# Performance work log

Hardware: AMD Instinct MI355X
Metric: run time of the kernel (lower is better)

Reference implementation:

```python
import jax, jax.numpy as jnp
import numpy as np

NUM_HEADS = 16
ROPE_BASE = 10000.0


def _rope_tables(head_dim, seq_len, dtype=jnp.float32):
    # Half-split convention: rotate first half against second half.
    inv_freq = 1.0 / (ROPE_BASE ** (jnp.arange(0, head_dim, 2, dtype=dtype) / head_dim))
    pos = jnp.arange(seq_len, dtype=dtype)
    angles_half = jnp.einsum('s,d->sd', pos, inv_freq)          # (S, D/2)
    angles = jnp.concatenate([angles_half, angles_half], -1)     # (S, D)
    return jnp.cos(angles), jnp.sin(angles)


def _apply_rope(x, cos, sin):
    # x: (H, S, D); cos/sin: (S, D) broadcast over heads
    half = x.shape[-1] // 2
    x1, x2 = x[..., :half], x[..., half:]
    x_rot = jnp.concatenate([-x2, x1], axis=-1)
    return x * cos + x_rot * sin


def setup_inputs() -> dict:
    key = jax.random.key(0)
    S, E = 2048, 2048
    ks = jax.random.split(key, 9)
    sc = 0.02
    return {
        'x': jax.random.normal(ks[0], (S, E), jnp.float32),
        'Wq': jax.random.normal(ks[1], (E, E), jnp.float32) * sc,
        'bq': jax.random.normal(ks[2], (E,), jnp.float32) * sc,
        'Wk': jax.random.normal(ks[3], (E, E), jnp.float32) * sc,
        'bk': jax.random.normal(ks[4], (E,), jnp.float32) * sc,
        'Wv': jax.random.normal(ks[5], (E, E), jnp.float32) * sc,
        'bv': jax.random.normal(ks[6], (E,), jnp.float32) * sc,
        'Wo': jax.random.normal(ks[7], (E, E), jnp.float32) * sc,
        'bo': jax.random.normal(ks[8], (E,), jnp.float32) * sc,
    }


def reference(x, Wq, bq, Wk, bk, Wv, bv, Wo, bo):
    S, E = x.shape
    H = NUM_HEADS
    D = E // H
    scale = D ** 0.5
    cos, sin = _rope_tables(D, S, x.dtype)

    def proj(W, b):
        return (x @ W.T + b).reshape(S, H, D).transpose(1, 0, 2)  # (H, S, D)

    q = _apply_rope(proj(Wq, bq), cos, sin)
    k = _apply_rope(proj(Wk, bk), cos, sin)
    v = proj(Wv, bv)

    scores = jnp.einsum('hsd,htd->hst', q, k) / scale  # (H, S, S)
    attn = jax.nn.softmax(scores, axis=-1)
    out = jnp.einsum('hst,htd->hsd', attn, v)          # (H, S, D)
    # Faithful to the original's transpose(0,1).view(S,E) on a (1,H,S,D)
    # tensor: an in-order (head-major) flatten reinterpreted as (S, E).
    out = out.reshape(S, E)
    return out @ Wo.T + bo
```

## Files before the change

kernel.cpp:

```cpp
#include <hip/hip_runtime.h>

#define SDIM 2048
#define EDIM 2048
#define NHEAD 16
#define DHEAD 128

typedef __attribute__((ext_vector_type(8))) short short8;
typedef __attribute__((ext_vector_type(4))) float floatx4;

__device__ __forceinline__ float bf2f(ushort u) {
    union { uint i; float f; } v; v.i = ((uint)u) << 16; return v.f;
}
__device__ __forceinline__ ushort f2bf(float f) {
    union { float f; uint i; } v; v.f = f;
    uint r = v.i + 0x7fff + ((v.i >> 16) & 1);
    return (ushort)(r >> 16);
}

__device__ __forceinline__ void gload_lds16(const ushort* g, ushort* l) {
    __builtin_amdgcn_global_load_lds(
        (const __attribute__((address_space(1))) void*)g,
        (__attribute__((address_space(3))) void*)l, 16, 0, 0);
}

__global__ void convert5_kernel(
    const float* __restrict__ s0, const float* __restrict__ s1,
    const float* __restrict__ s2, const float* __restrict__ s3,
    const float* __restrict__ s4,
    ushort* __restrict__ d0, ushort* __restrict__ d1,
    ushort* __restrict__ d2, ushort* __restrict__ d3,
    ushort* __restrict__ d4)
{
    const float* src; ushort* dst;
    switch (blockIdx.y) {
        case 0: src = s0; dst = d0; break;
        case 1: src = s1; dst = d1; break;
        case 2: src = s2; dst = d2; break;
        case 3: src = s3; dst = d3; break;
        default: src = s4; dst = d4; break;
    }
    int i = blockIdx.x * blockDim.x + threadIdx.x;
    float4 f = ((const float4*)src)[i];
    ushort4 o;
    o.x = f2bf(f.x); o.y = f2bf(f.y); o.z = f2bf(f.z); o.w = f2bf(f.w);
    ((ushort4*)dst)[i] = o;
}

#define QPRESCALE 0.12754245f
__global__ void rope_kernel(ushort* __restrict__ Q, ushort* __restrict__ K) {
    int t = blockIdx.x * blockDim.x + threadIdx.x;
    int arr = t >> 18;
    int r = t & 0x3FFFF;
    int g = r & 7;
    int h = (r >> 3) & 15;
    int s = r >> 7;
    ushort* P = arr ? K : Q;
    float qsc = arr ? 1.0f : QPRESCALE;
    size_t base = ((size_t)s << 11) + (h << 7) + g * 8;
    union { uint4 v; ushort u[8]; } x1, x2, o1, o2;
    x1.v = *(const uint4*)(P + base);
    x2.v = *(const uint4*)(P + base + 64);
    float fs = (float)s;
#pragma unroll
    for (int j = 0; j < 8; j++) {
        int i = g * 8 + j;
        float inv = __expf((float)i * -0.14391157f);
        float ang = fs * inv;
        float rev = ang * 0.15915494309f;
        rev = rev - floorf(rev);
        float ar = rev * 6.28318530718f;
        float sn = __sinf(ar), cs = __cosf(ar);
        float a = bf2f(x1.u[j]), b = bf2f(x2.u[j]);
        o1.u[j] = f2bf((a * cs - b * sn) * qsc);
        o2.u[j] = f2bf((b * cs + a * sn) * qsc);
    }
    *(uint4*)(P + base) = o1.v;
    *(uint4*)(P + base + 64) = o2.v;
}

__device__ __forceinline__ void stout(float* p, float v)  { *p = v; }
__device__ __forceinline__ void stout(ushort* p, float v) { *p = f2bf(v); }

template <typename OUTT>
__global__ __launch_bounds__(256) void gemm_bt(
    const ushort* __restrict__ A,
    const ushort* __restrict__ B0, const ushort* __restrict__ B1, const ushort* __restrict__ B2,
    const float* __restrict__ s0, const float* __restrict__ s1, const float* __restrict__ s2,
    OUTT* __restrict__ C0, OUTT* __restrict__ C1, OUTT* __restrict__ C2,
    int nbpm, int vt_which)
{
    __shared__ __align__(16) ushort a_s[128 * 32];
    __shared__ __align__(16) ushort b_s[128 * 32];

    const int tid = threadIdx.x;
    const int wave = tid >> 6, lane = tid & 63;
    const int l15 = lane & 15, quad = lane >> 4;
    const int wm = wave & 1, wn = wave >> 1;
    const int bm = blockIdx.x * 128;
    const int which = blockIdx.y / nbpm;
    const int n0 = (blockIdx.y % nbpm) * 128;

    const ushort* B   = (which == 0) ? B0 : (which == 1) ? B1 : B2;
    const float*  bia = (which == 0) ? s0 : (which == 1) ? s1 : s2;
    OUTT*         C   = (which == 0) ? C0 : (which == 1) ? C1 : C2;

    floatx4 acc[4][4];
#pragma unroll
    for (int i = 0; i < 4; i++)
#pragma unroll
        for (int j = 0; j < 4; j++) acc[i][j] = (floatx4)0.0f;

    const int t1 = tid + 256;
    const int row0 = tid >> 2, kc0 = (tid & 3) * 8;
    const int row1 = t1 >> 2,  kc1 = (t1 & 3) * 8;

    for (int k0 = 0; k0 < EDIM; k0 += 32) {
        __syncthreads();
        gload_lds16(A + (size_t)(bm + row0) * EDIM + k0 + kc0, a_s + tid * 8);
        gload_lds16(A + (size_t)(bm + row1) * EDIM + k0 + kc1, a_s + t1 * 8);
        gload_lds16(B + (size_t)(n0 + row0) * EDIM + k0 + kc0, b_s + tid * 8);
        gload_lds16(B + (size_t)(n0 + row1) * EDIM + k0 + kc1, b_s + t1 * 8);
        __syncthreads();

        short8 af[4], bf[4];
#pragma unroll
        for (int mt = 0; mt < 4; mt++)
            af[mt] = *(const short8*)(a_s + (wm * 64 + mt * 16 + l15) * 32 + quad * 8);
#pragma unroll
        for (int nt = 0; nt < 4; nt++)
            bf[nt] = *(const short8*)(b_s + (wn * 64 + nt * 16 + l15) * 32 + quad * 8);
#pragma unroll
        for (int mt = 0; mt < 4; mt++)
#pragma unroll
            for (int nt = 0; nt < 4; nt++)
                acc[mt][nt] = __builtin_amdgcn_mfma_f32_16x16x32_bf16(af[mt], bf[nt], acc[mt][nt], 0, 0, 0);
    }

    if (which == vt_which) {
        ushort* Cv = (ushort*)C;
#pragma unroll
        for (int nt = 0; nt < 4; nt++) {
            int col = n0 + wn * 64 + nt * 16 + l15;
            int h = col >> 7, d = col & 127;
            float bv = bia[col];
#pragma unroll
            for (int mt = 0; mt < 4; mt++) {
                int s = bm + wm * 64 + mt * 16 + quad * 4;
                ushort4 pk;
                pk.x = f2bf(acc[mt][nt][0] + bv);
                pk.y = f2bf(acc[mt][nt][1] + bv);
                pk.z = f2bf(acc[mt][nt][2] + bv);
                pk.w = f2bf(acc[mt][nt][3] + bv);
                *(ushort4*)(Cv + (size_t)h * SDIM * DHEAD + (size_t)d * SDIM + s) = pk;
            }
        }
    } else {
#pragma unroll
        for (int nt = 0; nt < 4; nt++) {
            int col = n0 + wn * 64 + nt * 16 + l15;
            float bv = bia[col];
#pragma unroll
            for (int mt = 0; mt < 4; mt++) {
#pragma unroll
                for (int r = 0; r < 4; r++) {
                    int row = bm + wm * 64 + mt * 16 + quad * 4 + r;
                    stout(&C[(size_t)row * EDIM + col], acc[mt][nt][r] + bv);
                }
            }
        }
    }
}

#define MFIX2 17.31234049f
__global__ __launch_bounds__(256, 4) void attn_kernel(
    const ushort* __restrict__ Q, const ushort* __restrict__ K,
    const ushort* __restrict__ Vtg,
    ushort* __restrict__ Opart, float* __restrict__ Lsum,
    ushort* __restrict__ Ab, int nsplit)
{
    __shared__ __align__(16) ushort Ks[64 * 128];
    __shared__ __align__(16) ushort Vt[128 * 64];
    __shared__ __align__(16) ushort Ps[64 * 64];

    const int bid = blockIdx.x;
    const int head = bid & 15, qt = (bid >> 4) & 31, half = bid >> 9;
    const int tid = threadIdx.x, wave = tid >> 6, lane = tid & 63;
    const int l15 = lane & 15, quad = lane >> 4;
    const int l7 = l15 & 7;
    const int kstart = half * (SDIM / nsplit);
    const int ntile = (SDIM / nsplit) / 64;

    short8 qf[4];
    {
        int s = qt * 64 + wave * 16 + l15;
        const ushort* qp = Q + (size_t)s * EDIM + head * DHEAD;
#pragma unroll
        for (int kc = 0; kc < 4; kc++) qf[kc] = *(const short8*)(qp + kc * 32 + quad * 8);
    }

    floatx4 o[8];
#pragma unroll
    for (int i = 0; i < 8; i++) o[i] = (floatx4)0.0f;
    float lrow[4] = {0.f, 0.f, 0.f, 0.f};

    const int krow = tid >> 4, kc8 = tid & 15;
    const int vd = tid >> 3, vc8 = tid & 7;

    for (int kv = 0; kv < ntile; kv++) {
        const int k0 = kstart + kv * 64;
        __syncthreads();
#pragma unroll
        for (int i = 0; i < 4; i++) {
            int row = krow + i * 16;
            uint4 v = *(const uint4*)(K + (size_t)(k0 + row) * EDIM + head * DHEAD + kc8 * 8);
            *(uint4*)(Ks + row * 128 + ((kc8 ^ (row & 7)) << 3)) = v;
        }
#pragma unroll
        for (int i = 0; i < 4; i++) {
            int d = vd + i * 32;
            uint4 v = *(const uint4*)(Vtg + (size_t)head * SDIM * DHEAD + (size_t)d * SDIM + k0 + vc8 * 8);
            *(uint4*)(Vt + d * 64 + ((vc8 ^ (d & 7)) << 3)) = v;
        }
        __syncthreads();

        floatx4 sacc[4];
#pragma unroll
        for (int nt = 0; nt < 4; nt++) {
            sacc[nt] = (floatx4)0.0f;
#pragma unroll
            for (int kc = 0; kc < 4; kc++) {
                short8 bfr = *(const short8*)(Ks + (nt * 16 + l15) * 128 + (((kc * 4 + quad) ^ l7) << 3));
                sacc[nt] = __builtin_amdgcn_mfma_f32_16x16x32_bf16(qf[kc], bfr, sacc[nt], 0, 0, 0);
            }
        }

#pragma unroll
        for (int nt = 0; nt < 4; nt++) {
            int pcol8 = nt * 2 + (l15 >> 3);
#pragma unroll
            for (int r = 0; r < 4; r++) {
                float p = __builtin_amdgcn_exp2f(sacc[nt][r] - MFIX2);
                lrow[r] += p;
                int prow = wave * 16 + quad * 4 + r;
                Ps[prow * 64 + ((pcol8 ^ (prow & 7)) << 3) + l7] = f2bf(p);
            }
        }

#pragma unroll
        for (int kc2 = 0; kc2 < 2; kc2++) {
            int arow = wave * 16 + l15;
            short8 af = *(const short8*)(Ps + arow * 64 + (((kc2 * 4 + quad) ^ l7) << 3));
#pragma unroll
            for (int nt2 = 0; nt2 < 8; nt2++) {
                short8 bfr = *(const short8*)(Vt + (nt2 * 16 + l15) * 64 + (((kc2 * 4 + quad) ^ l7) << 3));
                o[nt2] = __builtin_amdgcn_mfma_f32_16x16x32_bf16(af, bfr, o[nt2], 0, 0, 0);
            }
        }
    }

#pragma unroll
    for (int r = 0; r < 4; r++) {
#pragma unroll
        for (int msk = 1; msk < 16; msk <<= 1)
            lrow[r] += __shfl_xor(lrow[r], msk, 16);
    }

    if (nsplit == 1) {
        float invl[4];
#pragma unroll
        for (int r = 0; r < 4; r++) invl[r] = 1.0f / lrow[r];
#pragma unroll
        for (int nt2 = 0; nt2 < 8; nt2++) {
#pragma unroll
            for (int r = 0; r < 4; r++) {
                int s = qt * 64 + wave * 16 + quad * 4 + r;
                int d = nt2 * 16 + l15;
                Ab[(size_t)head * SDIM * DHEAD + (size_t)s * DHEAD + d] = f2bf(o[nt2][r] * invl[r]);
            }
        }
    } else {
        size_t pb = ((size_t)half * NHEAD + head) * SDIM * DHEAD;
#pragma unroll
        for (int nt2 = 0; nt2 < 8; nt2++) {
#pragma unroll
            for (int r = 0; r < 4; r++) {
                int s = qt * 64 + wave * 16 + quad * 4 + r;
                int d = nt2 * 16 + l15;
                Opart[pb + (size_t)s * DHEAD + d] = f2bf(o[nt2][r]);
            }
        }
        if (l15 == 0) {
#pragma unroll
            for (int r = 0; r < 4; r++) {
                int s = qt * 64 + wave * 16 + quad * 4 + r;
                Lsum[((size_t)half * NHEAD + head) * SDIM + s] = lrow[r];
            }
        }
    }
}

__global__ void merge_kernel(const ushort* __restrict__ Opart,
                             const float* __restrict__ Lsum,
                             ushort* __restrict__ Ab)
{
    int t = blockIdx.x * blockDim.x + threadIdx.x;
    int row = t >> 4, c8 = (t & 15) * 8;
    float inv = 1.0f / (Lsum[row] + Lsum[NHEAD * SDIM + row]);
    union { uint4 v; ushort u[8]; } a0, a1, ro;
    a0.v = *(const uint4*)(Opart + (size_t)row * DHEAD + c8);
    a1.v = *(const uint4*)(Opart + (size_t)(NHEAD * SDIM) * DHEAD + (size_t)row * DHEAD + c8);
#pragma unroll
    for (int j = 0; j < 8; j++)
        ro.u[j] = f2bf((bf2f(a0.u[j]) + bf2f(a1.u[j])) * inv);
    *(uint4*)(Ab + (size_t)row * DHEAD + c8) = ro.v;
}

extern "C" void kernel_launch(void* const* d_in, const int* in_sizes, int n_in,
                              void* d_out, int out_size, void* d_ws, size_t ws_size,
                              hipStream_t stream) {
    (void)in_sizes; (void)n_in; (void)out_size;
    const float* x  = (const float*)d_in[0];
    const float* Wq = (const float*)d_in[1];
    const float* bq = (const float*)d_in[2];
    const float* Wk = (const float*)d_in[3];
    const float* bk = (const float*)d_in[4];
    const float* Wv = (const float*)d_in[5];
    const float* bv = (const float*)d_in[6];
    const float* Wo = (const float*)d_in[7];
    const float* bo = (const float*)d_in[8];
    float* out = (float*)d_out;

    char* ws = (char*)d_ws;
    const size_t SEG = (size_t)EDIM * EDIM * 2;
    ushort* xb  = (ushort*)(ws + 0 * SEG);
    ushort* Wqb = (ushort*)(ws + 1 * SEG);
    ushort* Wkb = (ushort*)(ws + 2 * SEG);
    ushort* Wvb = (ushort*)(ws + 3 * SEG);
    ushort* Wob = (ushort*)(ws + 4 * SEG);
    ushort* Qb  = (ushort*)(ws + 5 * SEG);
    ushort* Kb  = (ushort*)(ws + 6 * SEG);
    ushort* Vtg = (ushort*)(ws + 7 * SEG);
    ushort* Ab  = (ushort*)(ws + 8 * SEG);
    ushort* Op  = (ushort*)(ws + 9 * SEG);
    float*  Ls  = (float*)(ws + 11 * SEG);

    const int nsplit = (ws_size >= ((size_t)89 << 20)) ? 2 : 1;

    convert5_kernel<<<dim3(4096, 5), 256, 0, stream>>>(
        x, Wq, Wk, Wv, Wo, xb, Wqb, Wkb, Wvb, Wob);

    gemm_bt<ushort><<<dim3(16, 48), 256, 0, stream>>>(
        xb, Wqb, Wkb, Wvb, bq, bk, bv, Qb, Kb, Vtg, 16, 2);

    rope_kernel<<<2048, 256, 0, stream>>>(Qb, Kb);

    attn_kernel<<<512 * nsplit, 256, 0, stream>>>(Qb, Kb, Vtg, Op, Ls, Ab, nsplit);
    if (nsplit == 2)
        merge_kernel<<<2048, 256, 0, stream>>>(Op, Ls, Ab);

    gemm_bt<float><<<dim3(16, 16), 256, 0, stream>>>(
        Ab, Wob, Wob, Wob, bo, bo, bo, out, out, out, 16, -1);
}
```

Before: 336.5 us.

## Deepen GEMM K-step, remap blocks per XCD, transpose QK^T MFMA in attention

The GEMM now loads a 64-wide K slice per iteration, which halves the number of barrier pairs per block. It also launches a 1D grid that remaps block IDs so that blocks landing on the same XCD share M and N tiles, aiming for better L2 reuse. In the attention kernel, the S=K·Q^T MFMA operands are swapped so each lane holds a row's scores. This allows packed ushort4 stores of P, a single per-lane row sum, and a shorter shuffle reduction. The cost is double the LDS use in the GEMM and a block mapping that assumes the grid size divides evenly across 8 XCDs.

After: 347.4 us. 1.03x slower.

```diff
diff --git a/kernel.cpp b/kernel.cpp
--- a/kernel.cpp
+++ b/kernel.cpp
@@ -89,16 +89,22 @@
     OUTT* __restrict__ C0, OUTT* __restrict__ C1, OUTT* __restrict__ C2,
     int nbpm, int vt_which)
 {
-    __shared__ __align__(16) ushort a_s[128 * 32];
-    __shared__ __align__(16) ushort b_s[128 * 32];
+    __shared__ __align__(16) ushort a_s[2 * 128 * 32];
+    __shared__ __align__(16) ushort b_s[2 * 128 * 32];
 
     const int tid = threadIdx.x;
     const int wave = tid >> 6, lane = tid & 63;
     const int l15 = lane & 15, quad = lane >> 4;
     const int wm = wave & 1, wn = wave >> 1;
-    const int bm = blockIdx.x * 128;
-    const int which = blockIdx.y / nbpm;
-    const int n0 = (blockIdx.y % nbpm) * 128;
+
+    const int w = blockIdx.x;
+    const int xcd = w & 7, t = w >> 3;
+    const int Y = gridDim.x >> 4;
+    const int mtile = ((xcd & 1) << 3) | (t & 7);
+    const int y = (Y >> 2) * (xcd >> 1) + (t >> 3);
+    const int bm = mtile * 128;
+    const int which = y / nbpm;
+    const int n0 = (y % nbpm) * 128;
 
     const ushort* B   = (which == 0) ? B0 : (which == 1) ? B1 : B2;
     const float*  bia = (which == 0) ? s0 : (which == 1) ? s1 : s2;
@@ -110,30 +116,35 @@
 #pragma unroll
         for (int j = 0; j < 4; j++) acc[i][j] = (floatx4)0.0f;
 
-    const int t1 = tid + 256;
-    const int row0 = tid >> 2, kc0 = (tid & 3) * 8;
-    const int row1 = t1 >> 2,  kc1 = (t1 & 3) * 8;
-
-    for (int k0 = 0; k0 < EDIM; k0 += 32) {
+    for (int k0 = 0; k0 < EDIM; k0 += 64) {
         __syncthreads();
-        gload_lds16(A + (size_t)(bm + row0) * EDIM + k0 + kc0, a_s + tid * 8);
-        gload_lds16(A + (size_t)(bm + row1) * EDIM + k0 + kc1, a_s + t1 * 8);
-        gload_lds16(B + (size_t)(n0 + row0) * EDIM + k0 + kc0, b_s + tid * 8);
-        gload_lds16(B + (size_t)(n0 + row1) * EDIM + k0 + kc1, b_s + t1 * 8);
+#pragma unroll
+        for (int i = 0; i < 4; i++) {
+            int c = tid + i * 256;
+            int kk = c >> 9, row = (c >> 2) & 127, kin = (c & 3) * 8;
+            int gk = k0 + kk * 32 + kin;
+            gload_lds16(A + (size_t)(bm + row) * EDIM + gk, a_s + c * 8);
+            gload_lds16(B + (size_t)(n0 + row) * EDIM + gk, b_s + c * 8);
+        }
         __syncthreads();
 
-        short8 af[4], bf[4];
-#pragma unroll
-        for (int mt = 0; mt < 4; mt++)
-            af[mt] = *(const short8*)(a_s + (wm * 64 + mt * 16 + l15) * 32 + quad * 8);
-#pragma unroll
-        for (int nt = 0; nt < 4; nt++)
-            bf[nt] = *(const short8*)(b_s + (wn * 64 + nt * 16 + l15) * 32 + quad * 8);
-#pragma unroll
-        for (int mt = 0; mt < 4; mt++)
+#pragma unroll
+        for (int kk = 0; kk < 2; kk++) {
+            const ushort* ab = a_s + kk * 4096;
+            const ushort* bb = b_s + kk * 4096;
+            short8 af[4], bf[4];
+#pragma unroll
+            for (int mt = 0; mt < 4; mt++)
+                af[mt] = *(const short8*)(ab + (wm * 64 + mt * 16 + l15) * 32 + quad * 8);
 #pragma unroll
             for (int nt = 0; nt < 4; nt++)
-                acc[mt][nt] = __builtin_amdgcn_mfma_f32_16x16x32_bf16(af[mt], bf[nt], acc[mt][nt], 0, 0, 0);
+                bf[nt] = *(const short8*)(bb + (wn * 64 + nt * 16 + l15) * 32 + quad * 8);
+#pragma unroll
+            for (int mt = 0; mt < 4; mt++)
+#pragma unroll
+                for (int nt = 0; nt < 4; nt++)
+                    acc[mt][nt] = __builtin_amdgcn_mfma_f32_16x16x32_bf16(af[mt], bf[nt], acc[mt][nt], 0, 0, 0);
+        }
     }
 
     if (which == vt_which) {
@@ -201,10 +212,11 @@
     floatx4 o[8];
 #pragma unroll
     for (int i = 0; i < 8; i++) o[i] = (floatx4)0.0f;
-    float lrow[4] = {0.f, 0.f, 0.f, 0.f};
+    float lsum = 0.0f;
 
     const int krow = tid >> 4, kc8 = tid & 15;
     const int vd = tid >> 3, vc8 = tid & 7;
+    const int prow = wave * 16 + l15;
 
     for (int kv = 0; kv < ntile; kv++) {
         const int k0 = kstart + kv * 64;
@@ -223,33 +235,28 @@
         }
         __syncthreads();
 
-        floatx4 sacc[4];
 #pragma unroll
         for (int nt = 0; nt < 4; nt++) {
-            sacc[nt] = (floatx4)0.0f;
+            floatx4 st = (floatx4)0.0f;
 #pragma unroll
             for (int kc = 0; kc < 4; kc++) {
-                short8 bfr = *(const short8*)(Ks + (nt * 16 + l15) * 128 + (((kc * 4 + quad) ^ l7) << 3));
-                sacc[nt] = __builtin_amdgcn_mfma_f32_16x16x32_bf16(qf[kc], bfr, sacc[nt], 0, 0, 0);
-            }
-        }
-
-#pragma unroll
-        for (int nt = 0; nt < 4; nt++) {
-            int pcol8 = nt * 2 + (l15 >> 3);
-#pragma unroll
-            for (int r = 0; r < 4; r++) {
-                float p = __builtin_amdgcn_exp2f(sacc[nt][r] - MFIX2);
-                lrow[r] += p;
-                int prow = wave * 16 + quad * 4 + r;
-                Ps[prow * 64 + ((pcol8 ^ (prow & 7)) << 3) + l7] = f2bf(p);
-            }
+                short8 kfr = *(const short8*)(Ks + (nt * 16 + l15) * 128 + (((kc * 4 + quad) ^ l7) << 3));
+                st = __builtin_amdgcn_mfma_f32_16x16x32_bf16(kfr, qf[kc], st, 0, 0, 0);
+            }
+            ushort4 pk;
+            float p0 = __builtin_amdgcn_exp2f(st[0] - MFIX2);
+            float p1 = __builtin_amdgcn_exp2f(st[1] - MFIX2);
+            float p2 = __builtin_amdgcn_exp2f(st[2] - MFIX2);
+            float p3 = __builtin_amdgcn_exp2f(st[3] - MFIX2);
+            lsum += (p0 + p1) + (p2 + p3);
+            pk.x = f2bf(p0); pk.y = f2bf(p1); pk.z = f2bf(p2); pk.w = f2bf(p3);
+            int c2 = (nt * 2 + (quad >> 1)) ^ l7;
+            *(ushort4*)(Ps + prow * 64 + (c2 << 3) + ((quad & 1) << 2)) = pk;
         }
 
 #pragma unroll
         for (int kc2 = 0; kc2 < 2; kc2++) {
-            int arow = wave * 16 + l15;
-            short8 af = *(const short8*)(Ps + arow * 64 + (((kc2 * 4 + quad) ^ l7) << 3));
+            short8 af = *(const short8*)(Ps + prow * 64 + (((kc2 * 4 + quad) ^ l7) << 3));
 #pragma unroll
             for (int nt2 = 0; nt2 < 8; nt2++) {
                 short8 bfr = *(const short8*)(Vt + (nt2 * 16 + l15) * 64 + (((kc2 * 4 + quad) ^ l7) << 3));
@@ -258,17 +265,13 @@
         }
     }
 
-#pragma unroll
-    for (int r = 0; r < 4; r++) {
-#pragma unroll
-        for (int msk = 1; msk < 16; msk <<= 1)
-            lrow[r] += __shfl_xor(lrow[r], msk, 16);
-    }
+    lsum += __shfl_xor(lsum, 16);
+    lsum += __shfl_xor(lsum, 32);
 
     if (nsplit == 1) {
         float invl[4];
 #pragma unroll
-        for (int r = 0; r < 4; r++) invl[r] = 1.0f / lrow[r];
+        for (int r = 0; r < 4; r++) invl[r] = 1.0f / __shfl(lsum, quad * 4 + r, 16);
 #pragma unroll
         for (int nt2 = 0; nt2 < 8; nt2++) {
 #pragma unroll
@@ -289,13 +292,8 @@
                 Opart[pb + (size_t)s * DHEAD + d] = f2bf(o[nt2][r]);
             }
         }
-        if (l15 == 0) {
-#pragma unroll
-            for (int r = 0; r < 4; r++) {
-                int s = qt * 64 + wave * 16 + quad * 4 + r;
-                Lsum[((size_t)half * NHEAD + head) * SDIM + s] = lrow[r];
-            }
-        }
+        if (lane < 16)
+            Lsum[((size_t)half * NHEAD + head) * SDIM + qt * 64 + wave * 16 + lane] = lsum;
     }
 }
 
@@ -349,7 +347,7 @@
     convert5_kernel<<<dim3(4096, 5), 256, 0, stream>>>(
         x, Wq, Wk, Wv, Wo, xb, Wqb, Wkb, Wvb, Wob);
 
-    gemm_bt<ushort><<<dim3(16, 48), 256, 0, stream>>>(
+    gemm_bt<ushort><<<768, 256, 0, stream>>>(
         xb, Wqb, Wkb, Wvb, bq, bk, bv, Qb, Kb, Vtg, 16, 2);
 
     rope_kernel<<<2048, 256, 0, stream>>>(Qb, Kb);
@@ -358,6 +356,6 @@
     if (nsplit == 2)
         merge_kernel<<<2048, 256, 0, stream>>>(Op, Ls, Ab);
 
-    gemm_bt<float><<<dim3(16, 16), 256, 0, stream>>>(
+    gemm_bt<float><<<256, 256, 0, stream>>>(
         Ab, Wob, Wob, Wob, bo, bo, bo, out, out, out, 16, -1);
 }
```
